# Kernel tuning notes

Hardware: AMD Instinct MI355X
Metric: run time of the kernel (lower is better)

Reference implementation:

```python
import jax, jax.numpy as jnp
import numpy as np

HYP_C = 0.1
TAU = 0.1
MRG = 0.1
CLIP_R = 2.3
BS = 1024
NB_PROXIES = 256
SZ_EMBED = 128
T_BATCH = BS * 50
T_LCA = NB_PROXIES * 50


@jax.custom_vjp
def artanh(x):
    xc = jnp.clip(x, -1.0 + 1e-5, 1.0 - 1e-5)
    return 0.5 * (jnp.log1p(xc) - jnp.log1p(-xc))

def _artanh_fwd(x):
    xc = jnp.clip(x, -1.0 + 1e-5, 1.0 - 1e-5)
    return 0.5 * (jnp.log1p(xc) - jnp.log1p(-xc)), xc

def _artanh_bwd(xc, g):
    return (g / (1.0 - xc * xc),)

artanh.defvjp(_artanh_fwd, _artanh_bwd)


@jax.custom_vjp
def riemannian_fix(x):
    # identity fwd; bwd rescales euclidean grad to riemannian grad on the ball
    return x

def _riem_fwd(x):
    return x, x

def _riem_bwd(x, g):
    scale = ((1.0 - HYP_C * jnp.sum(x * x, axis=-1, keepdims=True)) ** 2) / 4.0
    return (g * scale,)

riemannian_fix.defvjp(_riem_fwd, _riem_bwd)


def expmap0(x, c):
    sqrt_c = c ** 0.5
    xn = jnp.maximum(jnp.linalg.norm(x, axis=-1, keepdims=True), 1e-5)
    return jnp.tanh(sqrt_c * xn) * x / (sqrt_c * xn)


def project(x, c):
    norm = jnp.maximum(jnp.linalg.norm(x, axis=-1, keepdims=True), 1e-5)
    maxnorm = (1.0 - 1e-3) / (c ** 0.5)
    return jnp.where(norm > maxnorm, x / norm * maxnorm, x)


def to_poincare(x, c, clip_r):
    xn = jnp.linalg.norm(x, axis=-1, keepdims=True) + 1e-5
    x = x * jnp.minimum(jnp.ones_like(xn), clip_r / xn)
    return riemannian_fix(project(expmap0(x, c), c))


def dist_matrix(x, y, c):
    # ||mobius_add(-x, y)|| computed in closed form (same math as the [N,M,D]
    # num/denom construction in the torch code; num_{nm} = a*( -x_n ) + b*y_m).
    sqrt_c = c ** 0.5
    xy = -jnp.einsum('nd,md->nm', x, y)        # (-x) . y
    x2 = jnp.sum(x * x, axis=-1, keepdims=True)  # [N,1]
    y2t = jnp.sum(y * y, axis=-1)[None, :]       # [1,M]
    a = 1.0 + 2.0 * c * xy + c * y2t             # coeff of -x
    b = 1.0 - c * x2                             # coeff of y
    denom = 1.0 + 2.0 * c * xy + (c ** 2) * x2 * y2t
    num_sq = a * a * x2 + 2.0 * a * b * xy + b * b * y2t
    norm = jnp.sqrt(jnp.maximum(num_sq, 1e-12)) / jnp.abs(denom + 1e-5)
    return (2.0 / sqrt_c) * artanh(sqrt_c * norm)


def gumbel_softmax_hard(logits, g):
    # straight-through hard gumbel softmax (tau=1 as in F.gumbel_softmax default)
    y = jax.nn.softmax(logits + g, axis=-1)
    hard = jax.nn.one_hot(jnp.argmax(y, axis=-1), y.shape[-1], dtype=y.dtype)
    return y + jax.lax.stop_gradient(hard - y)


def compute_ghhc(cp_dist, trip, g):
    i, j, k = trip[0], trip[1], trip[2]
    di, dj, dk = cp_dist[i], cp_dist[j], cp_dist[k]   # [T,P] each
    max_ij = jnp.maximum(di, dj)
    p_ij = gumbel_softmax_hard(-max_ij / TAU, g[0])
    max_ijk = jnp.maximum(dk, max_ij)
    p_ijk = gumbel_softmax_hard(-max_ijk / TAU, g[1])
    diff_lca = (jnp.argmax(p_ij, -1) != jnp.argmax(p_ijk, -1)).astype(cp_dist.dtype)
    d_i_ij = jnp.sum(di * p_ij, axis=1)
    d_i_ijk = jnp.sum(di * p_ijk, axis=1)
    d_j_ij = jnp.sum(dj * p_ij, axis=1)
    d_j_ijk = jnp.sum(dj * p_ijk, axis=1)
    d_k_ij = jnp.sum(dk * p_ij, axis=1)
    d_k_ijk = jnp.sum(dk * p_ijk, axis=1)
    hc = (jax.nn.relu(d_i_ij - d_i_ijk + MRG)
          + jax.nn.relu(d_j_ij - d_j_ijk + MRG)
          + jax.nn.relu(d_k_ijk - d_k_ij + MRG))
    return jnp.mean(hc * diff_lca)


def hp_loss(z_s, t_s, lcas, trip1, trip2, trip3, trip4, g1, g2, g3, g4):
    bs = z_s.shape[0]
    lh = to_poincare(lcas, HYP_C, CLIP_R)
    all_nodes = jnp.concatenate([z_s, lh], axis=0)
    D = dist_matrix(all_nodes, all_nodes, HYP_C)
    t_all = jnp.concatenate([t_s, lh], axis=0)
    Dt = dist_matrix(t_all, t_all, HYP_C)
    loss = compute_ghhc(D[:bs, bs:], trip1, g1)
    loss = loss + compute_ghhc(D[bs:, bs:], trip2, g2)
    loss = loss + compute_ghhc(Dt[:bs, bs:], trip3, g3)
    loss = loss + compute_ghhc(Dt[bs:, bs:], trip4, g4)
    return loss


def setup_inputs() -> dict:
    key = jax.random.key(0)
    ks = jax.random.split(key, 12)
    z_s = jax.random.normal(ks[0], (BS, SZ_EMBED), dtype=jnp.float32)
    t_s = jax.random.normal(ks[1], (BS, SZ_EMBED), dtype=jnp.float32)
    y = jax.random.uniform(ks[2], (BS, 24), dtype=jnp.float32)
    # lcas param init: randn / sqrt(d) * clip_r * 0.9
    lcas = jax.random.normal(ks[3], (NB_PROXIES, SZ_EMBED), dtype=jnp.float32)
    lcas = lcas / np.sqrt(SZ_EMBED) * CLIP_R * 0.9
    trip1 = jax.random.randint(ks[4], (3, T_BATCH), 0, BS, dtype=jnp.int32)
    trip2 = jax.random.randint(ks[5], (3, T_LCA), 0, NB_PROXIES, dtype=jnp.int32)
    trip3 = jax.random.randint(ks[6], (3, T_BATCH), 0, BS, dtype=jnp.int32)
    trip4 = jax.random.randint(ks[7], (3, T_LCA), 0, NB_PROXIES, dtype=jnp.int32)
    g1 = jax.random.gumbel(ks[8], (2, T_BATCH, NB_PROXIES), dtype=jnp.float32)
    g2 = jax.random.gumbel(ks[9], (2, T_LCA, NB_PROXIES), dtype=jnp.float32)
    g3 = jax.random.gumbel(ks[10], (2, T_BATCH, NB_PROXIES), dtype=jnp.float32)
    g4 = jax.random.gumbel(ks[11], (2, T_LCA, NB_PROXIES), dtype=jnp.float32)
    return {"z_s": z_s, "t_s": t_s, "y": y, "lcas": lcas,
            "trip1": trip1, "trip2": trip2, "trip3": trip3, "trip4": trip4,
            "g1": g1, "g2": g2, "g3": g3, "g4": g4}


def reference(z_s, t_s, y, lcas, trip1, trip2, trip3, trip4, g1, g2, g3, g4):
    # y only feeds the detached numpy mining loop in the original; the mined
    # triplets are supplied precomputed (trip1..4), so y does not enter the math.
    return hp_loss(z_s, t_s, lcas, trip1, trip2, trip3, trip4, g1, g2, g3, g4)
```

## Files before the change

### kernel.cpp

```cpp
#include <hip/hip_runtime.h>
#include <cstddef>
#include <stdint.h>

#define HYP_C   0.1f
#define SQRT_C  0.31622776601683794f
#define CLIP_R  2.3f
#define MRG     0.1f
#define NPROX   256
#define DIM     128

#define OFF_LH   0
#define OFF_LHT  32768
#define OFF_LN2  65536
#define OFF_D1   65792
#define OFF_D2   327936
#define OFF_D3   393472

__global__ __launch_bounds__(128)
void to_poincare_kernel(const float* __restrict__ lcas,
                        float* __restrict__ ws,
                        float* __restrict__ out)
{
    const int row = blockIdx.x;
    const int k   = threadIdx.x;
    if (row == 0 && k == 0) out[0] = 0.0f;

    float v  = lcas[row * DIM + k];
    float ss = v * v;
    #pragma unroll
    for (int off = 32; off >= 1; off >>= 1)
        ss += __shfl_xor(ss, off, 64);
    __shared__ float wpart[2];
    if ((k & 63) == 0) wpart[k >> 6] = ss;
    __syncthreads();
    const float sumsq = wpart[0] + wpart[1];

    const float s1 = sqrtf(sumsq);
    const float xn = s1 + 1e-5f;
    const float f1 = fminf(1.0f, CLIP_R / xn);
    const float xn2 = fmaxf(f1 * s1, 1e-5f);
    const float th  = tanhf(SQRT_C * xn2);
    const float f2  = th / (SQRT_C * xn2);
    const float nr      = fmaxf(f2 * f1 * s1, 1e-5f);
    const float maxnorm = (1.0f - 1e-3f) / SQRT_C;
    const float f3      = (nr > maxnorm) ? (maxnorm / nr) : 1.0f;

    const float f  = f3 * f2 * f1;
    const float lv = f * v;
    ws[OFF_LH  + row * DIM + k]   = lv;
    ws[OFF_LHT + k * NPROX + row] = lv;
    if (k == 0) ws[OFF_LN2 + row] = f * f * sumsq;
}

__global__ __launch_bounds__(256)
void dist_all_kernel(const float* __restrict__ z,
                     const float* __restrict__ t,
                     float* __restrict__ ws, int nb1)
{
    const float* lhT = ws + OFF_LHT;
    const float* ln2 = ws + OFF_LN2;

    int b = blockIdx.x;
    const float* X; float* Dout; int row0;
    if (b < nb1)            { X = z;            Dout = ws + OFF_D1; row0 = b * 4; }
    else if (b < nb1 + 64)  { X = ws + OFF_LH;  Dout = ws + OFF_D2; row0 = (b - nb1) * 4; }
    else                    { X = t;            Dout = ws + OFF_D3; row0 = (b - nb1 - 64) * 4; }

    __shared__ float xs[4][DIM];
    __shared__ float sx2[4];

    for (int idx = threadIdx.x; idx < 4 * DIM; idx += 256)
        xs[idx / DIM][idx % DIM] = X[row0 * DIM + idx];
    __syncthreads();

    const int wid  = threadIdx.x >> 6;
    const int lane = threadIdx.x & 63;
    {
        float a = xs[wid][lane];
        float c = xs[wid][lane + 64];
        float s = a * a + c * c;
        #pragma unroll
        for (int off = 32; off >= 1; off >>= 1)
            s += __shfl_xor(s, off, 64);
        if (lane == 0) sx2[wid] = s;
    }
    __syncthreads();

    const int m = threadIdx.x;
    float dot0 = 0.f, dot1 = 0.f, dot2 = 0.f, dot3 = 0.f;
    #pragma unroll 8
    for (int k = 0; k < DIM; k += 4) {
        const float4 x0 = *(const float4*)&xs[0][k];
        const float4 x1 = *(const float4*)&xs[1][k];
        const float4 x2 = *(const float4*)&xs[2][k];
        const float4 x3 = *(const float4*)&xs[3][k];
        const float l0 = lhT[(k + 0) * NPROX + m];
        const float l1 = lhT[(k + 1) * NPROX + m];
        const float l2 = lhT[(k + 2) * NPROX + m];
        const float l3 = lhT[(k + 3) * NPROX + m];
        dot0 = fmaf(x0.x, l0, fmaf(x0.y, l1, fmaf(x0.z, l2, fmaf(x0.w, l3, dot0))));
        dot1 = fmaf(x1.x, l0, fmaf(x1.y, l1, fmaf(x1.z, l2, fmaf(x1.w, l3, dot1))));
        dot2 = fmaf(x2.x, l0, fmaf(x2.y, l1, fmaf(x2.z, l2, fmaf(x2.w, l3, dot2))));
        dot3 = fmaf(x3.x, l0, fmaf(x3.y, l1, fmaf(x3.z, l2, fmaf(x3.w, l3, dot3))));
    }

    const float y2 = ln2[m];
    float dots[4] = {dot0, dot1, dot2, dot3};
    #pragma unroll
    for (int r = 0; r < 4; ++r) {
        const float x2 = sx2[r];
        const float xy = -dots[r];
        const float a  = 1.0f + 2.0f * HYP_C * xy + HYP_C * y2;
        const float bb = 1.0f - HYP_C * x2;
        const float denom  = 1.0f + 2.0f * HYP_C * xy + HYP_C * HYP_C * x2 * y2;
        const float num_sq = a * a * x2 + 2.0f * a * bb * xy + bb * bb * y2;
        const float nrm = sqrtf(fmaxf(num_sq, 1e-12f)) / fabsf(denom + 1e-5f);
        float u = SQRT_C * nrm;
        u = fminf(fmaxf(u, -1.0f + 1e-5f), 1.0f - 1e-5f);
        const float d = (2.0f / SQRT_C) * (0.5f * (log1pf(u) - log1pf(-u)));
        Dout[(size_t)(row0 + r) * NPROX + m] = d;
    }
}

__device__ __forceinline__ float dpp_fmax16(float x) {
    int o;
    o = __builtin_amdgcn_update_dpp(0, __float_as_int(x), 0x121, 0xF, 0xF, true);
    x = fmaxf(x, __int_as_float(o));
    o = __builtin_amdgcn_update_dpp(0, __float_as_int(x), 0x122, 0xF, 0xF, true);
    x = fmaxf(x, __int_as_float(o));
    o = __builtin_amdgcn_update_dpp(0, __float_as_int(x), 0x124, 0xF, 0xF, true);
    x = fmaxf(x, __int_as_float(o));
    o = __builtin_amdgcn_update_dpp(0, __float_as_int(x), 0x128, 0xF, 0xF, true);
    x = fmaxf(x, __int_as_float(o));
    return x;
}

__device__ __forceinline__ int dpp_imin16(int x) {
    int o;
    o = __builtin_amdgcn_update_dpp(0, x, 0x121, 0xF, 0xF, true); x = min(x, o);
    o = __builtin_amdgcn_update_dpp(0, x, 0x122, 0xF, 0xF, true); x = min(x, o);
    o = __builtin_amdgcn_update_dpp(0, x, 0x124, 0xF, 0xF, true); x = min(x, o);
    o = __builtin_amdgcn_update_dpp(0, x, 0x128, 0xF, 0xF, true); x = min(x, o);
    return x;
}

__global__ __launch_bounds__(256)
void ghhc_fused_kernel(const float* __restrict__ Da, const float* __restrict__ Db,
                       const float* __restrict__ Dc, const float* __restrict__ Dd,
                       const int* __restrict__ ta, const int* __restrict__ tb,
                       const int* __restrict__ tc, const int* __restrict__ td,
                       const float* __restrict__ ga, const float* __restrict__ gb,
                       const float* __restrict__ gc, const float* __restrict__ gd,
                       int Ta, int Tb, int Tc, int Td,
                       float sa, float sb, float sc_, float sd,
                       int nba, int nbb, int nbc,
                       float* __restrict__ out)
{
    const int tid = threadIdx.x;
    const int w   = tid >> 6;
    const int grp = (tid >> 4) & 3;
    const int hl  = tid & 15;
    const int hl4 = hl << 2;

    const int b = blockIdx.x;
    const float* D; const int* tr; const float* g; int Tt; float sc; int lb;
    if (b < nba)                   { D = Da; tr = ta; g = ga; Tt = Ta; sc = sa;  lb = b; }
    else if (b < nba + nbb)        { D = Db; tr = tb; g = gb; Tt = Tb; sc = sb;  lb = b - nba; }
    else if (b < nba + nbb + nbc)  { D = Dc; tr = tc; g = gc; Tt = Tc; sc = sc_; lb = b - nba - nbb; }
    else                           { D = Dd; tr = td; g = gd; Tt = Td; sc = sd;  lb = b - nba - nbb - nbc; }

    const int tstart = lb * 64 + w * 16;

    int iIt[4], jIt[4], kIt[4]; bool okIt[4];
    #pragma unroll
    for (int it = 0; it < 4; ++it) {
        int t = tstart + it * 4 + grp;
        okIt[it] = (t < Tt);
        t = okIt[it] ? t : (Tt - 1);
        iIt[it] = tr[t]; jIt[it] = tr[Tt + t]; kIt[it] = tr[2 * Tt + t];
    }

    float acc = 0.0f;

    #pragma unroll 1
    for (int it = 0; it < 4; ++it) {
        int t = tstart + it * 4 + grp;
        t = okIt[it] ? t : (Tt - 1);
        const int i = iIt[it], j = jIt[it], kk = kIt[it];

        const float4* Di = (const float4*)(D + (size_t)i  * NPROX);
        const float4* Dj = (const float4*)(D + (size_t)j  * NPROX);
        const float4* Dk = (const float4*)(D + (size_t)kk * NPROX);
        const float4* G0 = (const float4*)(g + (size_t)t * NPROX);
        const float4* G1 = (const float4*)(g + ((size_t)Tt + t) * NPROX);

        float dif[16], djf[16], dkf[16], g0f[16], g1f[16];
        #pragma unroll
        for (int m = 0; m < 4; ++m) {
            const int q = m * 16 + hl;
            float4 v;
            v = Di[q]; dif[m*4+0]=v.x; dif[m*4+1]=v.y; dif[m*4+2]=v.z; dif[m*4+3]=v.w;
            v = Dj[q]; djf[m*4+0]=v.x; djf[m*4+1]=v.y; djf[m*4+2]=v.z; djf[m*4+3]=v.w;
            v = Dk[q]; dkf[m*4+0]=v.x; dkf[m*4+1]=v.y; dkf[m*4+2]=v.z; dkf[m*4+3]=v.w;
            v = G0[q]; g0f[m*4+0]=v.x; g0f[m*4+1]=v.y; g0f[m*4+2]=v.z; g0f[m*4+3]=v.w;
            v = G1[q]; g1f[m*4+0]=v.x; g1f[m*4+1]=v.y; g1f[m*4+2]=v.z; g1f[m*4+3]=v.w;
        }

        float Sf[16], Uf[16];
        #pragma unroll
        for (int c = 0; c < 16; ++c) {
            const float m1 = fmaxf(dif[c], djf[c]);
            Sf[c] = fmaf(m1, -10.0f, g0f[c]);
            const float m2 = fmaxf(dkf[c], m1);
            Uf[c] = fmaf(m2, -10.0f, g1f[c]);
        }

        float lvA = Sf[0], lvB = Uf[0];
        #pragma unroll
        for (int c = 1; c < 16; ++c) { lvA = fmaxf(lvA, Sf[c]); lvB = fmaxf(lvB, Uf[c]); }
        const float gvA = dpp_fmax16(lvA);
        const float gvB = dpp_fmax16(lvB);

        int slA = 64, slB = 64;
        float pAi = -1.f, pAj = -1.f, pAk = -1.f;
        float pBi = -1.f, pBj = -1.f, pBk = -1.f;
        #pragma unroll
        for (int c = 15; c >= 0; --c) {
            const bool mA = (Sf[c] == gvA);
            slA = mA ? c : slA;
            pAi = mA ? dif[c] : pAi; pAj = mA ? djf[c] : pAj; pAk = mA ? dkf[c] : pAk;
            const bool mB = (Uf[c] == gvB);
            slB = mB ? c : slB;
            pBi = mB ? dif[c] : pBi; pBj = mB ? djf[c] : pBj; pBk = mB ? dkf[c] : pBk;
        }

        const int eA = (slA < 16) ? (((slA & 12) << 4) | (hl4 | (slA & 3))) : 1024;
        const int eB = (slB < 16) ? (((slB & 12) << 4) | (hl4 | (slB & 3))) : 1024;
        const int Ag = dpp_imin16(eA);
        const int Bg = dpp_imin16(eB);

        const bool ownA = (eA == Ag);
        const bool ownB = (eB == Bg);
        const float diA = dpp_fmax16(ownA ? pAi : -1.f);
        const float djA = dpp_fmax16(ownA ? pAj : -1.f);
        const float dkA = dpp_fmax16(ownA ? pAk : -1.f);
        const float diB = dpp_fmax16(ownB ? pBi : -1.f);
        const float djB = dpp_fmax16(ownB ? pBj : -1.f);
        const float dkB = dpp_fmax16(ownB ? pBk : -1.f);

        const float hc = fmaxf(diA - diB + MRG, 0.0f)
                       + fmaxf(djA - djB + MRG, 0.0f)
                       + fmaxf(dkB - dkA + MRG, 0.0f);
        acc += (okIt[it] && (Ag != Bg) && (hl == 0)) ? hc * sc : 0.0f;
    }

    acc += __shfl_xor(acc, 16, 64);
    acc += __shfl_xor(acc, 32, 64);
    __shared__ float wsum[4];
    if ((tid & 63) == 0) wsum[w] = acc;
    __syncthreads();
    if (tid == 0)
        atomicAdd(out, wsum[0] + wsum[1] + wsum[2] + wsum[3]);
}

extern "C" void kernel_launch(void* const* d_in, const int* in_sizes, int n_in,
                              void* d_out, int out_size, void* d_ws, size_t ws_size,
                              hipStream_t stream)
{
    const float* z_s  = (const float*)d_in[0];
    const float* t_s  = (const float*)d_in[1];
    const float* lcas = (const float*)d_in[3];
    const int* trip1 = (const int*)d_in[4];
    const int* trip2 = (const int*)d_in[5];
    const int* trip3 = (const int*)d_in[6];
    const int* trip4 = (const int*)d_in[7];
    const float* g1 = (const float*)d_in[8];
    const float* g2 = (const float*)d_in[9];
    const float* g3 = (const float*)d_in[10];
    const float* g4 = (const float*)d_in[11];
    float* out = (float*)d_out;
    float* ws  = (float*)d_ws;

    const int T1 = in_sizes[4] / 3;
    const int T2 = in_sizes[5] / 3;
    const int T3 = in_sizes[6] / 3;
    const int T4 = in_sizes[7] / 3;
    const int BS = in_sizes[0] / DIM;
    const int nb1 = BS / 4;

    to_poincare_kernel<<<NPROX, 128, 0, stream>>>(lcas, ws, out);

    dist_all_kernel<<<2 * nb1 + 64, 256, 0, stream>>>(z_s, t_s, ws, nb1);

    const int nbA = (T1 + 63) / 64;
    const int nbB = (T2 + 63) / 64;
    const int nbC = (T3 + 63) / 64;
    const int nbD = (T4 + 63) / 64;
    ghhc_fused_kernel<<<nbA + nbB + nbC + nbD, 256, 0, stream>>>(
        ws + OFF_D1, ws + OFF_D2, ws + OFF_D3, ws + OFF_D2,
        trip1, trip2, trip3, trip4,
        g1, g2, g3, g4,
        T1, T2, T3, T4,
        1.0f / (float)T1, 1.0f / (float)T2, 1.0f / (float)T3, 1.0f / (float)T4,
        nbA, nbB, nbC,
        out);
}
```

Baseline: 300.8 us.

## Software-pipeline triplet loads and gather winner distances instead of DPP reductions

Result: no change. 298.7 us (-0.7%).

```diff
diff --git a/kernel.cpp b/kernel.cpp
--- a/kernel.cpp
+++ b/kernel.cpp
@@ -144,7 +144,7 @@
     return x;
 }
 
-__global__ __launch_bounds__(256)
+__global__ __launch_bounds__(256, 3)
 void ghhc_fused_kernel(const float* __restrict__ Da, const float* __restrict__ Db,
                        const float* __restrict__ Dc, const float* __restrict__ Dd,
                        const int* __restrict__ ta, const int* __restrict__ tb,
@@ -171,41 +171,43 @@
 
     const int tstart = lb * 64 + w * 16;
 
-    int iIt[4], jIt[4], kIt[4]; bool okIt[4];
+    int iIt[4], jIt[4], kIt[4], tIt[4]; bool okIt[4];
     #pragma unroll
     for (int it = 0; it < 4; ++it) {
         int t = tstart + it * 4 + grp;
         okIt[it] = (t < Tt);
         t = okIt[it] ? t : (Tt - 1);
+        tIt[it] = t;
         iIt[it] = tr[t]; jIt[it] = tr[Tt + t]; kIt[it] = tr[2 * Tt + t];
     }
 
+    float dif[16], djf[16], dkf[16], g0f[16], g1f[16];
+
+    #define ISSUE(IT) { \
+        const float4* Di_ = (const float4*)(D + (size_t)iIt[IT] * NPROX); \
+        const float4* Dj_ = (const float4*)(D + (size_t)jIt[IT] * NPROX); \
+        const float4* Dk_ = (const float4*)(D + (size_t)kIt[IT] * NPROX); \
+        const float4* G0_ = (const float4*)(g + (size_t)tIt[IT] * NPROX); \
+        const float4* G1_ = (const float4*)(g + ((size_t)Tt + tIt[IT]) * NPROX); \
+        _Pragma("unroll") \
+        for (int m_ = 0; m_ < 4; ++m_) { \
+            const int q_ = m_ * 16 + hl; \
+            float4 v_; \
+            v_ = Di_[q_]; dif[m_*4+0]=v_.x; dif[m_*4+1]=v_.y; dif[m_*4+2]=v_.z; dif[m_*4+3]=v_.w; \
+            v_ = Dj_[q_]; djf[m_*4+0]=v_.x; djf[m_*4+1]=v_.y; djf[m_*4+2]=v_.z; djf[m_*4+3]=v_.w; \
+            v_ = Dk_[q_]; dkf[m_*4+0]=v_.x; dkf[m_*4+1]=v_.y; dkf[m_*4+2]=v_.z; dkf[m_*4+3]=v_.w; \
+            v_ = G0_[q_]; g0f[m_*4+0]=v_.x; g0f[m_*4+1]=v_.y; g0f[m_*4+2]=v_.z; g0f[m_*4+3]=v_.w; \
+            v_ = G1_[q_]; g1f[m_*4+0]=v_.x; g1f[m_*4+1]=v_.y; g1f[m_*4+2]=v_.z; g1f[m_*4+3]=v_.w; \
+        } }
+
     float acc = 0.0f;
-
-    #pragma unroll 1
+    float pdiA = 0.f, pdjA = 0.f, pdkA = 0.f, pdiB = 0.f, pdjB = 0.f, pdkB = 0.f;
+    bool  pC = false;
+
+    ISSUE(0);
+
+    #pragma unroll
     for (int it = 0; it < 4; ++it) {
-        int t = tstart + it * 4 + grp;
-        t = okIt[it] ? t : (Tt - 1);
-        const int i = iIt[it], j = jIt[it], kk = kIt[it];
-
-        const float4* Di = (const float4*)(D + (size_t)i  * NPROX);
-        const float4* Dj = (const float4*)(D + (size_t)j  * NPROX);
-        const float4* Dk = (const float4*)(D + (size_t)kk * NPROX);
-        const float4* G0 = (const float4*)(g + (size_t)t * NPROX);
-        const float4* G1 = (const float4*)(g + ((size_t)Tt + t) * NPROX);
-
-        float dif[16], djf[16], dkf[16], g0f[16], g1f[16];
-        #pragma unroll
-        for (int m = 0; m < 4; ++m) {
-            const int q = m * 16 + hl;
-            float4 v;
-            v = Di[q]; dif[m*4+0]=v.x; dif[m*4+1]=v.y; dif[m*4+2]=v.z; dif[m*4+3]=v.w;
-            v = Dj[q]; djf[m*4+0]=v.x; djf[m*4+1]=v.y; djf[m*4+2]=v.z; djf[m*4+3]=v.w;
-            v = Dk[q]; dkf[m*4+0]=v.x; dkf[m*4+1]=v.y; dkf[m*4+2]=v.z; dkf[m*4+3]=v.w;
-            v = G0[q]; g0f[m*4+0]=v.x; g0f[m*4+1]=v.y; g0f[m*4+2]=v.z; g0f[m*4+3]=v.w;
-            v = G1[q]; g1f[m*4+0]=v.x; g1f[m*4+1]=v.y; g1f[m*4+2]=v.z; g1f[m*4+3]=v.w;
-        }
-
         float Sf[16], Uf[16];
         #pragma unroll
         for (int c = 0; c < 16; ++c) {
@@ -215,6 +217,10 @@
             Uf[c] = fmaf(m2, -10.0f, g1f[c]);
         }
 
+        if (it == 0)      ISSUE(1)
+        else if (it == 1) ISSUE(2)
+        else if (it == 2) ISSUE(3)
+
         float lvA = Sf[0], lvB = Uf[0];
         #pragma unroll
         for (int c = 1; c < 16; ++c) { lvA = fmaxf(lvA, Sf[c]); lvB = fmaxf(lvB, Uf[c]); }
@@ -222,36 +228,42 @@
         const float gvB = dpp_fmax16(lvB);
 
         int slA = 64, slB = 64;
-        float pAi = -1.f, pAj = -1.f, pAk = -1.f;
-        float pBi = -1.f, pBj = -1.f, pBk = -1.f;
         #pragma unroll
         for (int c = 15; c >= 0; --c) {
-            const bool mA = (Sf[c] == gvA);
-            slA = mA ? c : slA;
-            pAi = mA ? dif[c] : pAi; pAj = mA ? djf[c] : pAj; pAk = mA ? dkf[c] : pAk;
-            const bool mB = (Uf[c] == gvB);
-            slB = mB ? c : slB;
-            pBi = mB ? dif[c] : pBi; pBj = mB ? djf[c] : pBj; pBk = mB ? dkf[c] : pBk;
+            slA = (Sf[c] == gvA) ? c : slA;
+            slB = (Uf[c] == gvB) ? c : slB;
         }
-
         const int eA = (slA < 16) ? (((slA & 12) << 4) | (hl4 | (slA & 3))) : 1024;
         const int eB = (slB < 16) ? (((slB & 12) << 4) | (hl4 | (slB & 3))) : 1024;
         const int Ag = dpp_imin16(eA);
         const int Bg = dpp_imin16(eB);
 
-        const bool ownA = (eA == Ag);
-        const bool ownB = (eB == Bg);
-        const float diA = dpp_fmax16(ownA ? pAi : -1.f);
-        const float djA = dpp_fmax16(ownA ? pAj : -1.f);
-        const float dkA = dpp_fmax16(ownA ? pAk : -1.f);
-        const float diB = dpp_fmax16(ownB ? pBi : -1.f);
-        const float djB = dpp_fmax16(ownB ? pBj : -1.f);
-        const float dkB = dpp_fmax16(ownB ? pBk : -1.f);
-
-        const float hc = fmaxf(diA - diB + MRG, 0.0f)
-                       + fmaxf(djA - djB + MRG, 0.0f)
-                       + fmaxf(dkB - dkA + MRG, 0.0f);
-        acc += (okIt[it] && (Ag != Bg) && (hl == 0)) ? hc * sc : 0.0f;
+        const float* Ri = D + (size_t)iIt[it] * NPROX;
+        const float* Rj = D + (size_t)jIt[it] * NPROX;
+        const float* Rk = D + (size_t)kIt[it] * NPROX;
+        const float eDiA = Ri[Ag], eDiB = Ri[Bg];
+        const float eDjA = Rj[Ag], eDjB = Rj[Bg];
+        const float eDkA = Rk[Ag], eDkB = Rk[Bg];
+
+        if (it > 0) {
+            const float hc = fmaxf(pdiA - pdiB + MRG, 0.0f)
+                           + fmaxf(pdjA - pdjB + MRG, 0.0f)
+                           + fmaxf(pdkB - pdkA + MRG, 0.0f);
+            acc += (pC && (hl == 0)) ? hc * sc : 0.0f;
+        }
+
+        pdiA = eDiA; pdiB = eDiB;
+        pdjA = eDjA; pdjB = eDjB;
+        pdkA = eDkA; pdkB = eDkB;
+        pC = okIt[it] && (Ag != Bg);
+    }
+    #undef ISSUE
+
+    {
+        const float hc = fmaxf(pdiA - pdiB + MRG, 0.0f)
+                       + fmaxf(pdjA - pdjB + MRG, 0.0f)
+                       + fmaxf(pdkB - pdkA + MRG, 0.0f);
+        acc += (pC && (hl == 0)) ? hc * sc : 0.0f;
     }
 
     acc += __shfl_xor(acc, 16, 64);
```
